# Performance work log

Measured on AMD Instinct MI355X. Metric: run time of the kernel, lower is better.

## Reference

```python
import jax, jax.numpy as jnp
import numpy as np
import math

NUM_CONVS = 4
GN_GROUPS = 32
GN_EPS = 1e-5
FPN_STRIDES = (8, 16, 32, 64, 128)
PRIOR_PROB = 0.01


def conv3x3(x, w, b):
    # x: [N,C,H,W], w: [O,I,3,3]
    y = jax.lax.conv_general_dilated(
        x, w, window_strides=(1, 1), padding='SAME',
        dimension_numbers=('NCHW', 'OIHW', 'NCHW'))
    return y + b[None, :, None, None]


def group_norm(x, gamma, beta):
    n, c, h, w = x.shape
    xg = x.reshape(n, GN_GROUPS, c // GN_GROUPS, h, w)
    mean = xg.mean(axis=(2, 3, 4), keepdims=True)
    var = xg.var(axis=(2, 3, 4), keepdims=True)
    xn = ((xg - mean) * jax.lax.rsqrt(var + GN_EPS)).reshape(n, c, h, w)
    return xn * gamma[None, :, None, None] + beta[None, :, None, None]


def subnet(x, ws, bs, gws, gbs):
    # NUM_CONVS x (conv3x3 -> GN -> ReLU)
    for i in range(NUM_CONVS):
        x = jax.nn.relu(group_norm(conv3x3(x, ws[i], bs[i]), gws[i], gbs[i]))
    return x


def permute_to_N_HWA_K(x, k):
    n = x.shape[0]
    return x.transpose(0, 2, 3, 1).reshape(n, -1, k)


def setup_inputs() -> dict:
    key = jax.random.key(0)
    ks = jax.random.split(key, 16)
    C, K = 256, 80
    feats = {
        'p3': jax.random.normal(ks[0], (1, C, 80, 80), jnp.float32),
        'p4': jax.random.normal(ks[1], (1, C, 40, 40), jnp.float32),
        'p5': jax.random.normal(ks[2], (1, C, 20, 20), jnp.float32),
        'p6': jax.random.normal(ks[3], (1, C, 10, 10), jnp.float32),
        'p7': jax.random.normal(ks[4], (1, C, 5, 5), jnp.float32),
    }
    std = 0.01
    bias_value = -math.log((1 - PRIOR_PROB) / PRIOR_PROB)
    params = {
        'cls_w': std * jax.random.normal(ks[5], (NUM_CONVS, C, C, 3, 3), jnp.float32),
        'cls_b': jnp.zeros((NUM_CONVS, C), jnp.float32),
        'cls_gn_w': jnp.ones((NUM_CONVS, C), jnp.float32),
        'cls_gn_b': jnp.zeros((NUM_CONVS, C), jnp.float32),
        'box_w': std * jax.random.normal(ks[6], (NUM_CONVS, C, C, 3, 3), jnp.float32),
        'box_b': jnp.zeros((NUM_CONVS, C), jnp.float32),
        'box_gn_w': jnp.ones((NUM_CONVS, C), jnp.float32),
        'box_gn_b': jnp.zeros((NUM_CONVS, C), jnp.float32),
        'score_w': std * jax.random.normal(ks[7], (K, C, 3, 3), jnp.float32),
        'score_b': jnp.full((K,), bias_value, jnp.float32),
        'pred_w': std * jax.random.normal(ks[8], (4, C, 3, 3), jnp.float32),
        'pred_b': jnp.zeros((4,), jnp.float32),
        'iou_w': std * jax.random.normal(ks[9], (1, C, 3, 3), jnp.float32),
        'iou_b': jnp.zeros((1,), jnp.float32),
        'scales': jnp.ones((5,), jnp.float32),
    }
    return {**feats, **params}


def reference(p3, p4, p5, p6, p7,
              cls_w, cls_b, cls_gn_w, cls_gn_b,
              box_w, box_b, box_gn_w, box_gn_b,
              score_w, score_b, pred_w, pred_b, iou_w, iou_b, scales):
    features = [p3, p4, p5, p6, p7]
    logits, bbox_reg, ious = [], [], []
    for l, feat in enumerate(features):
        c = subnet(feat, cls_w, cls_b, cls_gn_w, cls_gn_b)
        b = subnet(feat, box_w, box_b, box_gn_w, box_gn_b)
        logit = conv3x3(c, score_w, score_b)          # [N,80,H,W]
        iou = conv3x3(b, iou_w, iou_b)                # [N,1,H,W]
        bp = conv3x3(b, pred_w, pred_b) * scales[l]   # Scale module
        # norm_reg_targets=True branch
        reg = jax.nn.relu(bp) * FPN_STRIDES[l]        # [N,4,H,W]
        logits.append(permute_to_N_HWA_K(logit, 80))
        bbox_reg.append(permute_to_N_HWA_K(reg, 4))
        ious.append(permute_to_N_HWA_K(iou, 1))
    box_cls = jnp.concatenate(logits, axis=1)    # [N, sumHW, 80]
    box_delta = jnp.concatenate(bbox_reg, axis=1)  # [N, sumHW, 4]
    box_iou = jnp.concatenate(ious, axis=1)      # [N, sumHW, 1]
    # pack into one array for a single output: [N, sumHW, 85]
    return jnp.concatenate([box_cls, box_delta, box_iou], axis=-1)
```

## Files before the change

### kernel.cpp

```cpp
#include <hip/hip_runtime.h>

typedef unsigned short u16;
typedef __attribute__((ext_vector_type(8))) short bf16x8;
typedef __attribute__((ext_vector_type(4))) float f32x4;

#define NLEV 5
#define CCH 256
#define KTOT 2304
#define P_TOT 8525
#define PP_TOT 9165
#define PLS (PP_TOT*64)
#define HSTR 11776

__constant__ int   c_HW[NLEV]     = {6400, 1600, 400, 100, 25};
__constant__ int   c_W[NLEV]      = {80, 40, 20, 10, 5};
__constant__ int   c_off[NLEV]    = {0, 6400, 8000, 8400, 8500};
__constant__ int   c_poff[NLEV]   = {0, 6724, 8488, 8972, 9116};
__constant__ int   c_tls[NLEV+1]  = {0, 50, 65, 71, 73, 74};
__constant__ int   c_ntx[NLEV]    = {5, 3, 2, 1, 1};
__constant__ float c_stridef[NLEV]= {8.f, 16.f, 32.f, 64.f, 128.f};

__device__ __forceinline__ u16 f2bf(float f){
  union { float f; unsigned u; } v; v.f = f;
  unsigned r = v.u + 0x7fffu + ((v.u >> 16) & 1u);
  return (u16)(r >> 16);
}

__device__ __forceinline__ void g2l16(const u16* g, u16* l, int lane){
#if defined(__has_builtin)
#if __has_builtin(__builtin_amdgcn_global_load_lds)
  __builtin_amdgcn_global_load_lds(
      (const __attribute__((address_space(1))) unsigned int*)g,
      (__attribute__((address_space(3))) unsigned int*)l, 16, 0, 0);
  return;
#endif
#endif
  *(uint4*)(l + lane*8) = *(const uint4*)g;
}

#define WAIT_VM8   0x0F78
#define WAIT_VM0   0x0F70
#define WAIT_LGKM0 0xC07F

template<int MODE>
__global__ __launch_bounds__(256, 1) void gemm_conv(
    const u16* __restrict__ Xc, const u16* __restrict__ Xb,
    const u16* __restrict__ Wc, const u16* __restrict__ Wb,
    const float* __restrict__ bc, const float* __restrict__ bb,
    float* __restrict__ Yc, float* __restrict__ Yb,
    float* __restrict__ stats,
    const float* __restrict__ predb, const float* __restrict__ ioub,
    const float* __restrict__ scales, float* __restrict__ out)
{
  constexpr int NT = (MODE == 0) ? 8 : 4;
  __shared__ u16 hB[4*HSTR];
  __shared__ u16 sA[4][2][4096];
  __shared__ float sstat[32][2];

  const int ptile = blockIdx.x, br = blockIdx.z;
  int lv = 0;
  #pragma unroll
  for (int i = 1; i < NLEV; i++) if (ptile >= c_tls[i]) lv = i;
  const int tidx = ptile - c_tls[lv];
  const int ntx = c_ntx[lv];
  const int ty0 = (tidx / ntx) * 8, tx0 = (tidx - (tidx / ntx) * ntx) * 16;
  const int W = c_W[lv], wrow2 = W + 2;

  const int tid = threadIdx.x, wv = tid >> 6, ln = tid & 63;
  const int quad = ln >> 4, l15 = ln & 15;

  const u16* __restrict__ X  = br ? Xb : Xc;
  const u16* __restrict__ WA = br ? Wb : Wc;

  const int ASTR = (MODE == 0) ? 16384 : 8192;
  const u16* abase = WA + (size_t)(((MODE == 0) ? wv : (wv & 1)) * 8) * 512 + ln*8;

  const u16* hptr[6]; int hnum = 0;
  #pragma unroll
  for (int i = 0; i < 6; i++) {
    const int j = wv + 4*i;
    if (j < 23) {
      const int item = j*64 + ln;
      int hp = item >> 3; if (hp >= 180) hp -= 180;
      const int g = item & 7;
      const int hy = hp / 18, hx = hp - hy*18;
      const int prow = c_poff[lv] + (ty0 + hy)*wrow2 + tx0 + hx;
      hptr[i] = X + (size_t)prow*64 + ((g ^ (hp & 7)) << 3);
      hnum = i + 1;
    }
  }

  auto stageA = [&](int s, int b) {
    const u16* as = abase + (size_t)s * ASTR;
    u16* da = &sA[wv][b][0];
    #pragma unroll
    for (int j = 0; j < 8; j++) g2l16(as + j*512, da + j*512, ln);
  };

  f32x4 acc[4][NT];
  #pragma unroll
  for (int i = 0; i < 4; i++)
    #pragma unroll
    for (int j = 0; j < NT; j++) acc[i][j] = (f32x4){0.f, 0.f, 0.f, 0.f};

  if (MODE == 0 && tid < 64) sstat[tid >> 1][tid & 1] = 0.f;

  for (int i = 0; i < hnum; i++) {
    const int j = wv + 4*i;
    #pragma unroll
    for (int cc = 0; cc < 4; cc++)
      g2l16(hptr[i] + (size_t)cc*PLS, hB + cc*HSTR + j*512, ln);
  }
  stageA(0, 0);
  __syncthreads();
  stageA(4, 1);

  #pragma unroll 1
  for (int t = 0; t < 36; t++) {
    if (t < 35) __builtin_amdgcn_s_waitcnt(WAIT_VM8);
    else        __builtin_amdgcn_s_waitcnt(WAIT_VM0);
    const int cc = t / 9, tap = t - cc*9;
    const int dh = tap / 3, dw = tap - dh*3;
    const u16* myA = &sA[wv][t & 1][0];
    const u16* hpl = &hB[cc * HSTR];
    bf16x8 af[2][4], bf[2][NT];
    #pragma unroll
    for (int sub = 0; sub < 2; sub++) {
      const int q = sub*4 + quad;
      const int swzA = (q ^ (l15 & 7)) * 8;
      #pragma unroll
      for (int mt = 0; mt < 4; mt++)
        af[sub][mt] = *(const bf16x8*)&myA[(mt*16 + l15)*64 + swzA];
      #pragma unroll
      for (int nt = 0; nt < NT; nt++) {
        const int py = (MODE == 0) ? nt : ((wv >> 1)*4 + nt);
        const int hp = (py + dh)*18 + l15 + dw;
        bf[sub][nt] = *(const bf16x8*)&hpl[hp*64 + ((q ^ (hp & 7)) << 3)];
      }
    }
    __builtin_amdgcn_s_waitcnt(WAIT_LGKM0);
    if (t + 2 < 36) {
      const int t2 = t + 2, cc2 = t2 / 9, tap2 = t2 - cc2*9;
      stageA(tap2*4 + cc2, t & 1);
    }
    #pragma unroll
    for (int sub = 0; sub < 2; sub++)
      #pragma unroll
      for (int mt = 0; mt < 4; mt++)
        #pragma unroll
        for (int nt = 0; nt < NT; nt++)
          acc[mt][nt] = __builtin_amdgcn_mfma_f32_16x16x32_bf16(
              af[sub][mt], bf[sub][nt], acc[mt][nt], 0, 0, 0);
  }

  const int gx = tx0 + l15;
  if (MODE == 0) {
    const float* __restrict__ bias = br ? bb : bc;
    float* __restrict__ Y = br ? Yb : Yc;
    #pragma unroll
    for (int mt = 0; mt < 4; mt++) {
      const int mrow = wv*64 + mt*16 + quad*4;
      const f32x4 bv = *(const f32x4*)&bias[mrow];
      float s = 0.f, sq = 0.f;
      #pragma unroll
      for (int nt = 0; nt < NT; nt++) {
        const int gy = ty0 + nt;
        f32x4 v = acc[mt][nt] + bv;
        if (gy < W && gx < W) {
          const size_t n = (size_t)(c_off[lv] + gy*W + gx);
          *(f32x4*)&Y[n*CCH + mrow] = v;
          #pragma unroll
          for (int r = 0; r < 4; r++) { s += v[r]; sq += v[r]*v[r]; }
        }
      }
      #pragma unroll
      for (int o = 1; o < 16; o <<= 1) { s += __shfl_xor(s, o); sq += __shfl_xor(sq, o); }
      if (l15 == 0) {
        const int g = mrow >> 3;
        atomicAdd(&sstat[g][0], s);
        atomicAdd(&sstat[g][1], sq);
      }
    }
    __syncthreads();
    if (tid < 64) {
      const int g = tid >> 1, c = tid & 1;
      atomicAdd(&stats[((br*NLEV + lv)*32 + g)*2 + c], sstat[g][c]);
    }
  } else {
    const float scl = scales[lv];
    const float stf = c_stridef[lv];
    #pragma unroll
    for (int mt = 0; mt < 4; mt++) {
      const int mr0 = (wv & 1)*64 + mt*16 + quad*4;
      if (mr0 >= 85) continue;
      #pragma unroll
      for (int nt = 0; nt < NT; nt++) {
        const int gy = ty0 + (wv >> 1)*4 + nt;
        if (gy >= W || gx >= W) continue;
        const size_t n = (size_t)(c_off[lv] + gy*W + gx);
        const f32x4 v = acc[mt][nt];
        #pragma unroll
        for (int r = 0; r < 4; r++) {
          const int m = mr0 + r;
          if (br == 0) {
            if (m < 80) out[n*85 + m] = v[r] + bc[m];
          } else {
            if (m < 4) {
              const float t = (v[r] + predb[m]) * scl;
              out[n*85 + 80 + m] = fmaxf(t, 0.f) * stf;
            } else if (m == 4) {
              out[n*85 + 84] = v[r] + ioub[0];
            }
          }
        }
      }
    }
  }
}

__global__ __launch_bounds__(256) void gn_relu(
    const float* __restrict__ Yc, const float* __restrict__ Yb,
    const float* __restrict__ stats,
    const float* __restrict__ gwc, const float* __restrict__ gbc,
    const float* __restrict__ gwb, const float* __restrict__ gbb,
    u16* __restrict__ Xc, u16* __restrict__ Xb)
{
  const int t = blockIdx.x * 256 + threadIdx.x;
  if (t >= 2 * P_TOT * 32) return;
  const int br = t / (P_TOT * 32);
  const int r  = t - br * (P_TOT * 32);
  const int pg = r >> 5;
  const int c0 = (r & 31) << 3;
  int lv = 0;
  #pragma unroll
  for (int i = 1; i < NLEV; i++) if (pg >= c_off[i]) lv = i;
  const int pl = pg - c_off[lv];
  const int Wl = c_W[lv];
  const int g = c0 >> 3;
  const float* st = &stats[(((size_t)br*NLEV + lv)*32 + g)*2];
  const float cnt = 8.f * (float)c_HW[lv];
  const float mean = st[0] / cnt;
  const float var  = st[1] / cnt - mean*mean;
  const float rstd = rsqrtf(var + 1e-5f);
  const float* Y  = br ? Yb : Yc;
  const float* gw = br ? gwb : gwc;
  const float* gb = br ? gbb : gbc;
  u16* X = br ? Xb : Xc;
  const float* y = &Y[(size_t)pg*CCH + c0];
  const int h = pl / Wl, wi = pl - h*Wl;
  const size_t pidx = (size_t)(c_poff[lv] + (h+1)*(Wl+2) + (wi+1));
  union { u16 u[8]; uint4 v; } pk;
  #pragma unroll
  for (int i = 0; i < 8; i++) {
    const float v = (y[i] - mean)*rstd*gw[c0+i] + gb[c0+i];
    pk.u[i] = f2bf(fmaxf(v, 0.f));
  }
  *(uint4*)&X[(size_t)(c0 >> 6)*PLS + pidx*64 + (c0 & 63)] = pk.v;
}

__global__ __launch_bounds__(256) void feat2bf(
    const float* __restrict__ p3, const float* __restrict__ p4,
    const float* __restrict__ p5, const float* __restrict__ p6,
    const float* __restrict__ p7, u16* __restrict__ X)
{
  const int t = blockIdx.x * 256 + threadIdx.x;
  if (t >= P_TOT * 32) return;
  const int pg = t >> 5, c0 = (t & 31) << 3;
  int lv = 0;
  #pragma unroll
  for (int i = 1; i < NLEV; i++) if (pg >= c_off[i]) lv = i;
  const int pl = pg - c_off[lv];
  const float* src = lv==0 ? p3 : lv==1 ? p4 : lv==2 ? p5 : lv==3 ? p6 : p7;
  const int HW = c_HW[lv], Wl = c_W[lv];
  const int h = pl / Wl, wi = pl - h*Wl;
  const size_t pidx = (size_t)(c_poff[lv] + (h+1)*(Wl+2) + (wi+1));
  union { u16 u[8]; uint4 v; } pk;
  #pragma unroll
  for (int i = 0; i < 8; i++)
    pk.u[i] = f2bf(src[(size_t)(c0+i)*HW + pl]);
  *(uint4*)&X[(size_t)(c0 >> 6)*PLS + pidx*64 + (c0 & 63)] = pk.v;
}

__global__ __launch_bounds__(256) void wconv(
    const float* __restrict__ cw, const float* __restrict__ bw,
    u16* __restrict__ Wc, u16* __restrict__ Wb)
{
  const size_t N = (size_t)4*256*KTOT;
  const size_t t = (size_t)blockIdx.x * 256 + threadIdx.x;
  if (t >= 2*N) return;
  const float* src = (t < N) ? cw : bw;
  u16* dst = (t < N) ? Wc : Wb;
  const size_t i = (t < N) ? t : t - N;
  const size_t lc = i / KTOT;
  const int kk = (int)(i - lc*KTOT);
  const int l = (int)(lc >> 8), co = (int)(lc & 255);
  const int tap = kk >> 8, ci = kk & 255;
  const int s = kk >> 6, kl = kk & 63;
  const int r = co & 7, p = (kl >> 3) ^ r;
  const size_t d = (size_t)l*589824 +
      ((size_t)((s*32 + (co >> 3))*64 + r*8 + p))*8 + (kl & 7);
  dst[d] = f2bf(src[(lc*256 + ci)*9 + tap]);
}

__global__ __launch_bounds__(256) void hconv(
    const float* __restrict__ sw, const float* __restrict__ pw,
    const float* __restrict__ iw, u16* __restrict__ Whc, u16* __restrict__ Whb)
{
  const int N = 128 * KTOT;
  const int t = blockIdx.x * 256 + threadIdx.x;
  if (t >= 2*N) return;
  const int i = (t < N) ? t : t - N;
  const int co = i / KTOT, kk = i - co*KTOT;
  const int tap = kk >> 8, ci = kk & 255;
  const int s = kk >> 6, kl = kk & 63;
  const int r = co & 7, p = (kl >> 3) ^ r;
  const size_t d = ((size_t)((s*16 + (co >> 3))*64 + r*8 + p))*8 + (kl & 7);
  float v = 0.f;
  if (t < N) {
    if (co < 80) v = sw[(co*256 + ci)*9 + tap];
    Whc[d] = f2bf(v);
  } else {
    if (co < 4)       v = pw[(co*256 + ci)*9 + tap];
    else if (co == 4) v = iw[ci*9 + tap];
    Whb[d] = f2bf(v);
  }
}

extern "C" void kernel_launch(void* const* d_in, const int* in_sizes, int n_in,
                              void* d_out, int out_size, void* d_ws, size_t ws_size,
                              hipStream_t stream)
{
  const float* p3      = (const float*)d_in[0];
  const float* p4      = (const float*)d_in[1];
  const float* p5      = (const float*)d_in[2];
  const float* p6      = (const float*)d_in[3];
  const float* p7      = (const float*)d_in[4];
  const float* cls_w   = (const float*)d_in[5];
  const float* cls_b   = (const float*)d_in[6];
  const float* cls_gw  = (const float*)d_in[7];
  const float* cls_gb  = (const float*)d_in[8];
  const float* box_w   = (const float*)d_in[9];
  const float* box_b   = (const float*)d_in[10];
  const float* box_gw  = (const float*)d_in[11];
  const float* box_gb  = (const float*)d_in[12];
  const float* score_w = (const float*)d_in[13];
  const float* score_b = (const float*)d_in[14];
  const float* pred_w  = (const float*)d_in[15];
  const float* pred_b  = (const float*)d_in[16];
  const float* iou_w   = (const float*)d_in[17];
  const float* iou_b   = (const float*)d_in[18];
  const float* scales  = (const float*)d_in[19];
  float* out = (float*)d_out;

  char* w = (char*)d_ws;
  size_t o = 0;
  auto alloc = [&](size_t b) { void* p = w + o; o += (b + 255) & ~(size_t)255; return p; };
  u16*   XF = (u16*)alloc((size_t)PP_TOT*CCH*2);
  u16*   XC = (u16*)alloc((size_t)PP_TOT*CCH*2);
  u16*   XB = (u16*)alloc((size_t)PP_TOT*CCH*2);
  float* ST = (float*)alloc((size_t)4*2*NLEV*32*2*4);
  u16*  WRC = (u16*)alloc((size_t)4*256*KTOT*2);
  u16*  WRB = (u16*)alloc((size_t)4*256*KTOT*2);
  u16*  WHC = (u16*)alloc((size_t)128*KTOT*2);
  u16*  WHB = (u16*)alloc((size_t)128*KTOT*2);
  float* YC = (float*)alloc((size_t)P_TOT*CCH*4);
  float* YB = (float*)alloc((size_t)P_TOT*CCH*4);

  hipMemsetAsync(XF, 0, (size_t)3*PP_TOT*CCH*2 + (size_t)4*2*NLEV*32*2*4, stream);

  wconv<<<dim3((unsigned)(((size_t)2*4*256*KTOT + 255)/256)), 256, 0, stream>>>(cls_w, box_w, WRC, WRB);
  hconv<<<dim3((2*128*KTOT + 255)/256), 256, 0, stream>>>(score_w, pred_w, iou_w, WHC, WHB);
  feat2bf<<<dim3((P_TOT*32 + 255)/256), 256, 0, stream>>>(p3, p4, p5, p6, p7, XF);

  const u16* xci = XF; const u16* xbi = XF;
  for (int l = 0; l < 4; l++) {
    float* STl = ST + (size_t)l*2*NLEV*32*2;
    gemm_conv<0><<<dim3(74, 1, 2), 256, 0, stream>>>(
        xci, xbi, WRC + (size_t)l*589824, WRB + (size_t)l*589824,
        cls_b + l*256, box_b + l*256, YC, YB, STl,
        nullptr, nullptr, nullptr, nullptr);
    gn_relu<<<dim3((2*P_TOT*32 + 255)/256), 256, 0, stream>>>(
        YC, YB, STl, cls_gw + l*256, cls_gb + l*256, box_gw + l*256, box_gb + l*256,
        XC, XB);
    xci = XC; xbi = XB;
  }
  gemm_conv<1><<<dim3(74, 1, 2), 256, 0, stream>>>(
      xci, xbi, WHC, WHB, score_b, nullptr, nullptr, nullptr, nullptr,
      pred_b, iou_b, scales, out);
}
```

Before: 374.0 us.

## Split conv GEMM output channels across two blocks and double-buffer halo planes

Each trunk conv block now covers 128 output channels instead of 256, so the grid doubles (74x2x2) and each wave holds a 32x128 accumulator tile. The halo input is no longer staged all at once: it streams through two channel-chunk planes with barriers, which frees LDS and lets two blocks share a CU (launch_bounds 256,2). The aim is better occupancy and CU coverage on a small grid, at the cost of loading the input halo twice and adding sync points and finer waitcnt handling.

```diff
diff --git a/kernel.cpp b/kernel.cpp
--- a/kernel.cpp
+++ b/kernel.cpp
@@ -38,12 +38,13 @@
   *(uint4*)(l + lane*8) = *(const uint4*)g;
 }
 
-#define WAIT_VM8   0x0F78
+#define WAIT_VM4   0x0F74
+#define WAIT_VM10  0x0F7A
 #define WAIT_VM0   0x0F70
 #define WAIT_LGKM0 0xC07F
 
 template<int MODE>
-__global__ __launch_bounds__(256, 1) void gemm_conv(
+__global__ __launch_bounds__(256, 2) void gemm_conv(
     const u16* __restrict__ Xc, const u16* __restrict__ Xb,
     const u16* __restrict__ Wc, const u16* __restrict__ Wb,
     const float* __restrict__ bc, const float* __restrict__ bb,
@@ -52,12 +53,13 @@
     const float* __restrict__ predb, const float* __restrict__ ioub,
     const float* __restrict__ scales, float* __restrict__ out)
 {
-  constexpr int NT = (MODE == 0) ? 8 : 4;
-  __shared__ u16 hB[4*HSTR];
-  __shared__ u16 sA[4][2][4096];
-  __shared__ float sstat[32][2];
-
-  const int ptile = blockIdx.x, br = blockIdx.z;
+  __shared__ u16 hB[2*HSTR];
+  __shared__ u16 sA[4][2][2048];
+  __shared__ float sstat[16][2];
+
+  const int ptile = blockIdx.x;
+  const int mtile = (MODE == 0) ? blockIdx.y : 0;
+  const int br = blockIdx.z;
   int lv = 0;
   #pragma unroll
   for (int i = 1; i < NLEV; i++) if (ptile >= c_tls[i]) lv = i;
@@ -73,84 +75,95 @@
   const u16* __restrict__ WA = br ? Wb : Wc;
 
   const int ASTR = (MODE == 0) ? 16384 : 8192;
-  const u16* abase = WA + (size_t)(((MODE == 0) ? wv : (wv & 1)) * 8) * 512 + ln*8;
-
-  const u16* hptr[6]; int hnum = 0;
+  const u16* abase = WA +
+      (size_t)(((MODE == 0) ? mtile*16 : 0) + wv*4) * 512 + ln*8;
+
+  const u16* hptr[6]; int hslab[6];
   #pragma unroll
   for (int i = 0; i < 6; i++) {
-    const int j = wv + 4*i;
-    if (j < 23) {
-      const int item = j*64 + ln;
-      int hp = item >> 3; if (hp >= 180) hp -= 180;
-      const int g = item & 7;
-      const int hy = hp / 18, hx = hp - hy*18;
-      const int prow = c_poff[lv] + (ty0 + hy)*wrow2 + tx0 + hx;
-      hptr[i] = X + (size_t)prow*64 + ((g ^ (hp & 7)) << 3);
-      hnum = i + 1;
-    }
-  }
-
+    int j = wv + 4*i;
+    if (j > 22) j -= 4;
+    hslab[i] = j;
+    const int item = j*64 + ln;
+    int hp = item >> 3; if (hp >= 180) hp -= 180;
+    const int g = item & 7;
+    const int hy = hp / 18, hx = hp - hy*18;
+    const int prow = c_poff[lv] + (ty0 + hy)*wrow2 + tx0 + hx;
+    hptr[i] = X + (size_t)prow*64 + ((g ^ (hp & 7)) << 3);
+  }
+
+  auto stageH = [&](int plane) {
+    u16* dst = &hB[(plane & 1) * HSTR];
+    const size_t cof = (size_t)plane * PLS;
+    #pragma unroll
+    for (int i = 0; i < 6; i++)
+      g2l16(hptr[i] + cof, dst + hslab[i]*512, ln);
+  };
   auto stageA = [&](int s, int b) {
     const u16* as = abase + (size_t)s * ASTR;
     u16* da = &sA[wv][b][0];
     #pragma unroll
-    for (int j = 0; j < 8; j++) g2l16(as + j*512, da + j*512, ln);
+    for (int j = 0; j < 4; j++) g2l16(as + j*512, da + j*512, ln);
   };
 
-  f32x4 acc[4][NT];
-  #pragma unroll
-  for (int i = 0; i < 4; i++)
-    #pragma unroll
-    for (int j = 0; j < NT; j++) acc[i][j] = (f32x4){0.f, 0.f, 0.f, 0.f};
-
-  if (MODE == 0 && tid < 64) sstat[tid >> 1][tid & 1] = 0.f;
-
-  for (int i = 0; i < hnum; i++) {
-    const int j = wv + 4*i;
-    #pragma unroll
-    for (int cc = 0; cc < 4; cc++)
-      g2l16(hptr[i] + (size_t)cc*PLS, hB + cc*HSTR + j*512, ln);
-  }
+  f32x4 acc[2][8];
+  #pragma unroll
+  for (int i = 0; i < 2; i++)
+    #pragma unroll
+    for (int j = 0; j < 8; j++) acc[i][j] = (f32x4){0.f, 0.f, 0.f, 0.f};
+
+  if (MODE == 0 && tid < 32) sstat[tid >> 1][tid & 1] = 0.f;
+
+  stageH(0);
+  stageH(1);
   stageA(0, 0);
+  stageA(4, 1);
   __syncthreads();
-  stageA(4, 1);
-
+
+  int cc = 0, tap = 0;
   #pragma unroll 1
   for (int t = 0; t < 36; t++) {
-    if (t < 35) __builtin_amdgcn_s_waitcnt(WAIT_VM8);
-    else        __builtin_amdgcn_s_waitcnt(WAIT_VM0);
-    const int cc = t / 9, tap = t - cc*9;
+    if (t == 10 || t == 19) __builtin_amdgcn_s_waitcnt(WAIT_VM10);
+    else if (t == 35)       __builtin_amdgcn_s_waitcnt(WAIT_VM0);
+    else                    __builtin_amdgcn_s_waitcnt(WAIT_VM4);
+    if (tap == 0 && cc > 0) {
+      __builtin_amdgcn_sched_barrier(0);
+      __builtin_amdgcn_s_barrier();
+      __builtin_amdgcn_sched_barrier(0);
+      if (cc < 3) stageH(cc + 1);
+    }
+    const u16* myA = &sA[wv][t & 1][0];
+    const u16* hpl = &hB[(cc & 1) * HSTR];
     const int dh = tap / 3, dw = tap - dh*3;
-    const u16* myA = &sA[wv][t & 1][0];
-    const u16* hpl = &hB[cc * HSTR];
-    bf16x8 af[2][4], bf[2][NT];
+    bf16x8 af[2][2], bf[2][8];
     #pragma unroll
     for (int sub = 0; sub < 2; sub++) {
       const int q = sub*4 + quad;
       const int swzA = (q ^ (l15 & 7)) * 8;
       #pragma unroll
-      for (int mt = 0; mt < 4; mt++)
+      for (int mt = 0; mt < 2; mt++)
         af[sub][mt] = *(const bf16x8*)&myA[(mt*16 + l15)*64 + swzA];
       #pragma unroll
-      for (int nt = 0; nt < NT; nt++) {
-        const int py = (MODE == 0) ? nt : ((wv >> 1)*4 + nt);
-        const int hp = (py + dh)*18 + l15 + dw;
+      for (int nt = 0; nt < 8; nt++) {
+        const int hp = (nt + dh)*18 + l15 + dw;
         bf[sub][nt] = *(const bf16x8*)&hpl[hp*64 + ((q ^ (hp & 7)) << 3)];
       }
     }
     __builtin_amdgcn_s_waitcnt(WAIT_LGKM0);
-    if (t + 2 < 36) {
-      const int t2 = t + 2, cc2 = t2 / 9, tap2 = t2 - cc2*9;
+    if (t < 34) {
+      int tap2 = tap + 2, cc2 = cc;
+      if (tap2 >= 9) { tap2 -= 9; cc2++; }
       stageA(tap2*4 + cc2, t & 1);
     }
     #pragma unroll
     for (int sub = 0; sub < 2; sub++)
       #pragma unroll
-      for (int mt = 0; mt < 4; mt++)
+      for (int mt = 0; mt < 2; mt++)
         #pragma unroll
-        for (int nt = 0; nt < NT; nt++)
+        for (int nt = 0; nt < 8; nt++)
           acc[mt][nt] = __builtin_amdgcn_mfma_f32_16x16x32_bf16(
               af[sub][mt], bf[sub][nt], acc[mt][nt], 0, 0, 0);
+    if (++tap == 9) { tap = 0; cc++; }
   }
 
   const int gx = tx0 + l15;
@@ -158,12 +171,13 @@
     const float* __restrict__ bias = br ? bb : bc;
     float* __restrict__ Y = br ? Yb : Yc;
     #pragma unroll
-    for (int mt = 0; mt < 4; mt++) {
-      const int mrow = wv*64 + mt*16 + quad*4;
+    for (int mt = 0; mt < 2; mt++) {
+      const int mloc = wv*32 + mt*16 + quad*4;
+      const int mrow = mtile*128 + mloc;
       const f32x4 bv = *(const f32x4*)&bias[mrow];
       float s = 0.f, sq = 0.f;
       #pragma unroll
-      for (int nt = 0; nt < NT; nt++) {
+      for (int nt = 0; nt < 8; nt++) {
         const int gy = ty0 + nt;
         f32x4 v = acc[mt][nt] + bv;
         if (gy < W && gx < W) {
@@ -176,26 +190,26 @@
       #pragma unroll
       for (int o = 1; o < 16; o <<= 1) { s += __shfl_xor(s, o); sq += __shfl_xor(sq, o); }
       if (l15 == 0) {
-        const int g = mrow >> 3;
+        const int g = mloc >> 3;
         atomicAdd(&sstat[g][0], s);
         atomicAdd(&sstat[g][1], sq);
       }
     }
     __syncthreads();
-    if (tid < 64) {
+    if (tid < 32) {
       const int g = tid >> 1, c = tid & 1;
-      atomicAdd(&stats[((br*NLEV + lv)*32 + g)*2 + c], sstat[g][c]);
+      atomicAdd(&stats[((br*NLEV + lv)*32 + mtile*16 + g)*2 + c], sstat[g][c]);
     }
   } else {
     const float scl = scales[lv];
     const float stf = c_stridef[lv];
     #pragma unroll
-    for (int mt = 0; mt < 4; mt++) {
-      const int mr0 = (wv & 1)*64 + mt*16 + quad*4;
+    for (int mt = 0; mt < 2; mt++) {
+      const int mr0 = wv*32 + mt*16 + quad*4;
       if (mr0 >= 85) continue;
       #pragma unroll
-      for (int nt = 0; nt < NT; nt++) {
-        const int gy = ty0 + (wv >> 1)*4 + nt;
+      for (int nt = 0; nt < 8; nt++) {
+        const int gy = ty0 + nt;
         if (gy >= W || gx >= W) continue;
         const size_t n = (size_t)(c_off[lv] + gy*W + gx);
         const f32x4 v = acc[mt][nt];
@@ -375,7 +389,7 @@
   const u16* xci = XF; const u16* xbi = XF;
   for (int l = 0; l < 4; l++) {
     float* STl = ST + (size_t)l*2*NLEV*32*2;
-    gemm_conv<0><<<dim3(74, 1, 2), 256, 0, stream>>>(
+    gemm_conv<0><<<dim3(74, 2, 2), 256, 0, stream>>>(
         xci, xbi, WRC + (size_t)l*589824, WRB + (size_t)l*589824,
         cls_b + l*256, box_b + l*256, YC, YB, STl,
         nullptr, nullptr, nullptr, nullptr);
```

New measurement: 354.8 us. 5.2% less time.
